# Kernel tuning notes

Measured on AMD Instinct MI355X. Metric: run time of the kernel, lower is better.

The kernel has to match this reference:

```python
import jax, jax.numpy as jnp
import numpy as np

# Hard-coded constants from the original module
GAMMA = 0.1      # self.gamma default
N_STEPS = 10     # self.n_steps default
RHO = 0.9        # RMSProp decay
LR = 0.009       # RMSProp learning rate
MOM = 0.9        # momentum
EPS = 1e-8       # RMSProp epsilon
ABS_EPS = 1e-6   # diff_abs smoothing: diff_abs(x) = sqrt(x^2 + 1e-6)

B, IN_DIM, OUT_DIM = 4096, 2048, 4096


def setup_inputs() -> dict:
    key = jax.random.key(0)
    k1, k2 = jax.random.split(key)
    inputs = jax.random.normal(k1, (B, IN_DIM), dtype=jnp.float32)
    # keras 'uniform' init: U(-0.05, 0.05), shape (output_dim, input_dim)
    W = jax.random.uniform(k2, (OUT_DIM, IN_DIM), minval=-0.05, maxval=0.05, dtype=jnp.float32)
    return {"inputs": inputs, "W": W}


def reference(inputs, W):
    batch = inputs.shape[0]
    out_dim = W.shape[0]
    a = jnp.sqrt(inputs * inputs + ABS_EPS)          # diff_abs(inputs), [B, in_dim]
    act = lambda u: 0.5 * (1.0 + jnp.exp(-u))        # self.activation

    def cost(x):
        # l1_norm.sum() + l1_inov + own_norm  (prior = 0)
        l1 = (GAMMA * act(x @ W) * a).sum()
        l1_inov = (GAMMA / 10.0) * jnp.sum(x * x)
        own = GAMMA * jnp.sum(jnp.sqrt(x * x + ABS_EPS))
        return l1 + l1_inov + own

    grad_cost = jax.grad(cost)

    def step(carry, _):
        x, acc1, acc2 = carry
        g = grad_cost(x)                              # [B, out_dim]
        new_acc1 = RHO * acc1 + (1.0 - RHO) * g * g
        denom = jnp.sqrt(new_acc1 + EPS)
        new_acc2 = MOM * acc2 - LR * g / denom
        cand = x - LR * g / denom
        t = 0.1 * LR / denom                          # elementwise prox threshold
        new_x = jnp.maximum(cand - t, 0.0) + jnp.minimum(cand + t, 0.0) + MOM * new_acc2
        new_x = jax.lax.stop_gradient(new_x)          # theano disconnected_grad
        return (new_x, new_acc1, new_acc2), None

    z = jnp.zeros((batch, out_dim), dtype=inputs.dtype)
    # scan runs n_steps; last step's l1_norm uses the state after n_steps-1 updates,
    # so run n_steps-1 updates then compute the final l1_norm directly.
    (x, _, _), _ = jax.lax.scan(step, (z, z, z), None, length=N_STEPS - 1)
    return GAMMA * act(x @ W) * a                     # outputs[-1][-1]: last l1_norm, [B, in_dim]
```

## Files before the change

kernel.cpp:

```cpp
#include <hip/hip_runtime.h>
#include <cstdint>
#include <cstddef>

#define B_DIM   4096
#define IN_DIM  2048
#define OUT_DIM 4096

typedef __attribute__((ext_vector_type(8))) __bf16 bf16x8;
typedef __attribute__((ext_vector_type(4))) float  f32x4;

__device__ __forceinline__ unsigned short f2bf(float f) {
    unsigned int u = __float_as_uint(f);
    u += 0x7FFFu + ((u >> 16) & 1u);
    return (unsigned short)(u >> 16);
}
__device__ __forceinline__ float bf2f(unsigned short b) {
    return __uint_as_float(((unsigned int)b) << 16);
}

__device__ __forceinline__ void gload16(const void* g, void* l) {
    __builtin_amdgcn_global_load_lds(
        (const __attribute__((address_space(1))) void*)g,
        (__attribute__((address_space(3))) void*)l, 16, 0, 0);
}

__global__ void prep_g0_kernel(const float* __restrict__ in, unsigned short* __restrict__ Gb) {
    int i = blockIdx.x * 256 + threadIdx.x;
    float4 v = reinterpret_cast<const float4*>(in)[i];
    ushort4 g;
    g.x = f2bf(-0.05f * sqrtf(v.x * v.x + 1e-6f));
    g.y = f2bf(-0.05f * sqrtf(v.y * v.y + 1e-6f));
    g.z = f2bf(-0.05f * sqrtf(v.z * v.z + 1e-6f));
    g.w = f2bf(-0.05f * sqrtf(v.w * v.w + 1e-6f));
    reinterpret_cast<ushort4*>(Gb)[i] = g;
}

__global__ void conv_w_kernel(const float* __restrict__ W, unsigned short* __restrict__ Wb,
                              unsigned short* __restrict__ WTb) {
    __shared__ float tile[64][65];
    const int i0 = blockIdx.x * 64;
    const int j0 = blockIdx.y * 64;
    const int c  = threadIdx.x & 63;
    const int rq = threadIdx.x >> 6;
#pragma unroll
    for (int rp = 0; rp < 16; ++rp) {
        int row = rp * 4 + rq;
        float w = W[(size_t)(j0 + row) * IN_DIM + i0 + c];
        tile[row][c] = w;
        Wb[(size_t)(j0 + row) * IN_DIM + i0 + c] = f2bf(w);
    }
    __syncthreads();
#pragma unroll
    for (int rp = 0; rp < 16; ++rp) {
        int row = rp * 4 + rq;
        WTb[(size_t)(i0 + row) * OUT_DIM + j0 + c] = f2bf(tile[c][row]);
    }
}

template <int EPI>
__global__ __launch_bounds__(256, 2)
void gemm_nt(const unsigned short* __restrict__ A, const unsigned short* __restrict__ Bm,
             int N, int K,
             const float* __restrict__ inb, unsigned short* __restrict__ Gb,
             float* __restrict__ out,
             float* __restrict__ x, unsigned short* __restrict__ acc1,
             unsigned short* __restrict__ acc2, unsigned short* __restrict__ xb) {
    __shared__ alignas(16) char smem[17408];
    const int tid  = threadIdx.x;
    const int lane = tid & 63;
    const int w    = tid >> 6;
    const int nbx  = N >> 7;
    const int nwg  = gridDim.x;
    const int cpx  = nwg >> 3;
    const int bid  = (int)blockIdx.x;
    const int swz  = (bid & 7) * cpx + (bid >> 3);
    const int bx   = swz % nbx;
    const int by   = swz / nbx;
    const int row0 = by << 7;
    const int col0 = bx << 7;

    const int q     = lane >> 2;
    const int s     = lane & 3;
    const int rowS0 = w * 16 + q;
    const size_t strideK2 = (size_t)K * 2;
    const char* Ab = (const char*)A;
    const char* Bb = (const char*)Bm;
    const char* gA0 = Ab + (size_t)(row0 + rowS0)      * strideK2 + s * 16;
    const char* gA1 = Ab + (size_t)(row0 + rowS0 + 64) * strideK2 + s * 16;
    const char* gB0 = Bb + (size_t)(col0 + rowS0)      * strideK2 + s * 16;
    const char* gB1 = Bb + (size_t)(col0 + rowS0 + 64) * strideK2 + s * 16;
    char* lA0 = smem + w * 1024;
    char* lA1 = smem + 4096  + w * 1024;
    char* lB0 = smem + 8192  + w * 1024;
    char* lB1 = smem + 12288 + w * 1024;

    const int wm = w >> 1, wn = w & 1;
    int aOff[4], bOff[4];
#pragma unroll
    for (int m = 0; m < 4; ++m) {
        aOff[m] = (wm * 64 + m * 16 + (lane & 15)) * 64 + ((lane >> 4) * 16);
        bOff[m] = 8192 + (wn * 64 + m * 16 + (lane & 15)) * 64 + ((lane >> 4) * 16);
    }

    f32x4 acc[4][4] = {};

    for (int k0 = 0; k0 < K; k0 += 32) {
        const size_t kb = (size_t)k0 * 2;
        gload16(gA0 + kb, lA0);
        gload16(gA1 + kb, lA1);
        gload16(gB0 + kb, lB0);
        gload16(gB1 + kb, lB1);
        __syncthreads();
        bf16x8 aF[4], bF[4];
#pragma unroll
        for (int m = 0; m < 4; ++m) aF[m] = *reinterpret_cast<const bf16x8*>(smem + aOff[m]);
#pragma unroll
        for (int n = 0; n < 4; ++n) bF[n] = *reinterpret_cast<const bf16x8*>(smem + bOff[n]);
#pragma unroll
        for (int m = 0; m < 4; ++m)
#pragma unroll
            for (int n = 0; n < 4; ++n)
                acc[m][n] = __builtin_amdgcn_mfma_f32_16x16x32_bf16(aF[m], bF[n], acc[m][n], 0, 0, 0);
        __syncthreads();
    }

    float* lep = (float*)(smem + w * 4352);
    const int li = lane >> 4;
    const int lc = lane & 15;
    const int row0w = row0 + wm * 64;
    const int col0w = col0 + wn * 64;
#pragma unroll
    for (int m = 0; m < 4; ++m) {
#pragma unroll
        for (int n = 0; n < 4; ++n)
#pragma unroll
            for (int i = 0; i < 4; ++i)
                lep[(li * 4 + i) * 68 + n * 16 + lc] = acc[m][n][i];
#pragma unroll
        for (int rr = 0; rr < 4; ++rr) {
            const int row = rr + li * 4;
            float4 v = *reinterpret_cast<const float4*>(&lep[row * 68 + lc * 4]);
            const size_t idx  = (size_t)(row0w + m * 16 + row) * N + col0w + lc * 4;
            const size_t idx4 = idx >> 2;
            if constexpr (EPI == 0) {
                float4 iv = reinterpret_cast<const float4*>(inb)[idx4];
                ushort4 g;
                g.x = f2bf(-0.05f * sqrtf(iv.x * iv.x + 1e-6f) * expf(-v.x));
                g.y = f2bf(-0.05f * sqrtf(iv.y * iv.y + 1e-6f) * expf(-v.y));
                g.z = f2bf(-0.05f * sqrtf(iv.z * iv.z + 1e-6f) * expf(-v.z));
                g.w = f2bf(-0.05f * sqrtf(iv.w * iv.w + 1e-6f) * expf(-v.w));
                *reinterpret_cast<ushort4*>(&Gb[idx]) = g;
            } else if constexpr (EPI == 1) {
                float4 iv = reinterpret_cast<const float4*>(inb)[idx4];
                float4 o;
                o.x = 0.05f * (1.0f + expf(-v.x)) * sqrtf(iv.x * iv.x + 1e-6f);
                o.y = 0.05f * (1.0f + expf(-v.y)) * sqrtf(iv.y * iv.y + 1e-6f);
                o.z = 0.05f * (1.0f + expf(-v.z)) * sqrtf(iv.z * iv.z + 1e-6f);
                o.w = 0.05f * (1.0f + expf(-v.w)) * sqrtf(iv.w * iv.w + 1e-6f);
                reinterpret_cast<float4*>(out)[idx4] = o;
            } else {
                float4  xv  = reinterpret_cast<const float4*>(x)[idx4];
                ushort4 a1u = *reinterpret_cast<const ushort4*>(&acc1[idx]);
                ushort4 a2u = *reinterpret_cast<const ushort4*>(&acc2[idx]);
                float xs[4] = {xv.x, xv.y, xv.z, xv.w};
                float vs[4] = {v.x, v.y, v.z, v.w};
                unsigned short a1s[4] = {a1u.x, a1u.y, a1u.z, a1u.w};
                unsigned short a2s[4] = {a2u.x, a2u.y, a2u.z, a2u.w};
                float xn4[4]; unsigned short a1n[4], a2n[4], xbn[4];
#pragma unroll
                for (int j = 0; j < 4; ++j) {
                    float g    = vs[j] + 0.02f * xs[j] + 0.1f * xs[j] * rsqrtf(xs[j] * xs[j] + 1e-6f);
                    float a1   = 0.9f * bf2f(a1s[j]) + 0.1f * g * g;
                    float inv  = rsqrtf(a1 + 1e-8f);
                    float r_   = 0.009f * g * inv;
                    float a2   = 0.9f * bf2f(a2s[j]) - r_;
                    float cand = xs[j] - r_;
                    float t    = 0.0009f * inv;
                    float xn   = fmaxf(cand - t, 0.0f) + fminf(cand + t, 0.0f) + 0.9f * a2;
                    xn4[j] = xn; a1n[j] = f2bf(a1); a2n[j] = f2bf(a2); xbn[j] = f2bf(xn);
                }
                float4 xo = {xn4[0], xn4[1], xn4[2], xn4[3]};
                reinterpret_cast<float4*>(x)[idx4] = xo;
                *reinterpret_cast<ushort4*>(&acc1[idx]) = make_ushort4(a1n[0], a1n[1], a1n[2], a1n[3]);
                *reinterpret_cast<ushort4*>(&acc2[idx]) = make_ushort4(a2n[0], a2n[1], a2n[2], a2n[3]);
                *reinterpret_cast<ushort4*>(&xb[idx])   = make_ushort4(xbn[0], xbn[1], xbn[2], xbn[3]);
            }
        }
    }
}

extern "C" void kernel_launch(void* const* d_in, const int* in_sizes, int n_in,
                              void* d_out, int out_size, void* d_ws, size_t ws_size,
                              hipStream_t stream) {
    const float* in = (const float*)d_in[0];
    const float* W  = (const float*)d_in[1];
    float* out = (float*)d_out;
    char* ws = (char*)d_ws;

    float*          x    = (float*)(ws);
    unsigned short* acc1 = (unsigned short*)(ws + ((size_t)64  << 20));
    unsigned short* acc2 = (unsigned short*)(ws + ((size_t)96  << 20));
    unsigned short* xb   = (unsigned short*)(ws + ((size_t)128 << 20));
    unsigned short* Wb   = (unsigned short*)(ws + ((size_t)160 << 20));
    unsigned short* WTb  = (unsigned short*)(ws + ((size_t)176 << 20));
    unsigned short* Gb   = (unsigned short*)(ws + ((size_t)192 << 20));

    hipMemsetAsync(ws, 0, (size_t)128 << 20, stream);

    prep_g0_kernel<<<dim3(B_DIM * IN_DIM / 4 / 256), dim3(256), 0, stream>>>(in, Gb);
    conv_w_kernel<<<dim3(IN_DIM / 64, OUT_DIM / 64), dim3(256), 0, stream>>>(W, Wb, WTb);

    const int gridFwd  = (IN_DIM / 128) * (B_DIM / 128);
    const int gridGrad = (OUT_DIM / 128) * (B_DIM / 128);

    for (int step = 0; step < 9; ++step) {
        if (step > 0) {
            gemm_nt<0><<<dim3(gridFwd), dim3(256), 0, stream>>>(
                xb, WTb, IN_DIM, OUT_DIM, in, Gb, nullptr, nullptr, nullptr, nullptr, nullptr);
        }
        gemm_nt<2><<<dim3(gridGrad), dim3(256), 0, stream>>>(
            Gb, Wb, OUT_DIM, IN_DIM, nullptr, nullptr, nullptr, x, acc1, acc2, xb);
    }
    gemm_nt<1><<<dim3(gridFwd), dim3(256), 0, stream>>>(
        xb, WTb, IN_DIM, OUT_DIM, in, nullptr, out, nullptr, nullptr, nullptr, nullptr);
}
```

Before: 1.869 ms.

## Replace GEMM with larger-tile 4-stage ring-buffered pipeline using swizzled LDS

The bf16 GEMM is rewritten with 512-thread blocks and larger output tiles (128x256 forward, 256x256 grad). Global-to-LDS loads go through a 4-slot ring with prefetch three k-steps ahead and explicit vmcnt waits, replacing the old load-sync-compute-sync loop. The LDS layout is XOR-swizzled to avoid bank conflicts, and MFMA sections raise wave priority. This aims to hide memory latency and improve operand reuse, at the cost of much more LDS per block and lower occupancy.

```diff
diff --git a/kernel.cpp b/kernel.cpp
--- a/kernel.cpp
+++ b/kernel.cpp
@@ -8,13 +8,14 @@
 
 typedef __attribute__((ext_vector_type(8))) __bf16 bf16x8;
 typedef __attribute__((ext_vector_type(4))) float  f32x4;
-
-__device__ __forceinline__ unsigned short f2bf(float f) {
+typedef unsigned short ushortT;
+
+__device__ __forceinline__ ushortT f2bf(float f) {
     unsigned int u = __float_as_uint(f);
     u += 0x7FFFu + ((u >> 16) & 1u);
-    return (unsigned short)(u >> 16);
-}
-__device__ __forceinline__ float bf2f(unsigned short b) {
+    return (ushortT)(u >> 16);
+}
+__device__ __forceinline__ float bf2f(ushortT b) {
     return __uint_as_float(((unsigned int)b) << 16);
 }
 
@@ -24,7 +25,7 @@
         (__attribute__((address_space(3))) void*)l, 16, 0, 0);
 }
 
-__global__ void prep_g0_kernel(const float* __restrict__ in, unsigned short* __restrict__ Gb) {
+__global__ void prep_g0_kernel(const float* __restrict__ in, ushortT* __restrict__ Gb) {
     int i = blockIdx.x * 256 + threadIdx.x;
     float4 v = reinterpret_cast<const float4*>(in)[i];
     ushort4 g;
@@ -35,8 +36,8 @@
     reinterpret_cast<ushort4*>(Gb)[i] = g;
 }
 
-__global__ void conv_w_kernel(const float* __restrict__ W, unsigned short* __restrict__ Wb,
-                              unsigned short* __restrict__ WTb) {
+__global__ void conv_w_kernel(const float* __restrict__ W, ushortT* __restrict__ Wb,
+                              ushortT* __restrict__ WTb) {
     __shared__ float tile[64][65];
     const int i0 = blockIdx.x * 64;
     const int j0 = blockIdx.y * 64;
@@ -57,85 +58,145 @@
     }
 }
 
-template <int EPI>
-__global__ __launch_bounds__(256, 2)
-void gemm_nt(const unsigned short* __restrict__ A, const unsigned short* __restrict__ Bm,
-             int N, int K,
-             const float* __restrict__ inb, unsigned short* __restrict__ Gb,
-             float* __restrict__ out,
-             float* __restrict__ x, unsigned short* __restrict__ acc1,
-             unsigned short* __restrict__ acc2, unsigned short* __restrict__ xb) {
-    __shared__ alignas(16) char smem[17408];
+template <int EPI, int BM>
+__global__ __launch_bounds__(512, 2)
+void gemm_ring(const ushortT* __restrict__ A, const ushortT* __restrict__ Bm,
+               int N, int K,
+               const float* __restrict__ inb, ushortT* __restrict__ Gb,
+               float* __restrict__ out,
+               float* __restrict__ x, ushortT* __restrict__ acc1,
+               ushortT* __restrict__ acc2, ushortT* __restrict__ xb) {
+    constexpr int BN   = 256;
+    constexpr int ASZ  = BM * 64;
+    constexpr int BSZ  = BN * 64;
+    constexpr int SLOT = ASZ + BSZ;
+    constexpr int LA   = BM / 128;
+    constexpr int LB   = BN / 128;
+    constexpr int L    = LA + LB;
+    constexpr int MR   = BM / 32;
+    __shared__ alignas(16) char smem[4 * SLOT];
+
     const int tid  = threadIdx.x;
     const int lane = tid & 63;
     const int w    = tid >> 6;
-    const int nbx  = N >> 7;
+    const int wm   = w >> 2;
+    const int wn   = w & 3;
+    const int nbx  = N / BN;
     const int nwg  = gridDim.x;
     const int cpx  = nwg >> 3;
     const int bid  = (int)blockIdx.x;
     const int swz  = (bid & 7) * cpx + (bid >> 3);
     const int bx   = swz % nbx;
     const int by   = swz / nbx;
-    const int row0 = by << 7;
-    const int col0 = bx << 7;
-
-    const int q     = lane >> 2;
-    const int s     = lane & 3;
-    const int rowS0 = w * 16 + q;
+    const int row0 = by * BM;
+    const int col0 = bx * BN;
+
     const size_t strideK2 = (size_t)K * 2;
-    const char* Ab = (const char*)A;
-    const char* Bb = (const char*)Bm;
-    const char* gA0 = Ab + (size_t)(row0 + rowS0)      * strideK2 + s * 16;
-    const char* gA1 = Ab + (size_t)(row0 + rowS0 + 64) * strideK2 + s * 16;
-    const char* gB0 = Bb + (size_t)(col0 + rowS0)      * strideK2 + s * 16;
-    const char* gB1 = Bb + (size_t)(col0 + rowS0 + 64) * strideK2 + s * 16;
-    char* lA0 = smem + w * 1024;
-    char* lA1 = smem + 4096  + w * 1024;
-    char* lB0 = smem + 8192  + w * 1024;
-    char* lB1 = smem + 12288 + w * 1024;
-
-    const int wm = w >> 1, wn = w & 1;
-    int aOff[4], bOff[4];
-#pragma unroll
-    for (int m = 0; m < 4; ++m) {
-        aOff[m] = (wm * 64 + m * 16 + (lane & 15)) * 64 + ((lane >> 4) * 16);
-        bOff[m] = 8192 + (wn * 64 + m * 16 + (lane & 15)) * 64 + ((lane >> 4) * 16);
-    }
-
-    f32x4 acc[4][4] = {};
-
-    for (int k0 = 0; k0 < K; k0 += 32) {
-        const size_t kb = (size_t)k0 * 2;
-        gload16(gA0 + kb, lA0);
-        gload16(gA1 + kb, lA1);
-        gload16(gB0 + kb, lB0);
-        gload16(gB1 + kb, lB1);
-        __syncthreads();
+
+    const char* gAp[LA]; int lAo[LA];
+#pragma unroll
+    for (int i = 0; i < LA; ++i) {
+        int Lp  = i * 512 + tid;
+        int row = Lp >> 2, sl = Lp & 3;
+        int src = sl ^ ((row >> 1) & 3);
+        gAp[i] = (const char*)A + (size_t)(row0 + row) * strideK2 + src * 16;
+        lAo[i] = i * 8192 + w * 1024;
+    }
+    const char* gBp[LB]; int lBo[LB];
+#pragma unroll
+    for (int i = 0; i < LB; ++i) {
+        int Lp  = i * 512 + tid;
+        int row = Lp >> 2, sl = Lp & 3;
+        int src = sl ^ ((row >> 1) & 3);
+        gBp[i] = (const char*)Bm + (size_t)(col0 + row) * strideK2 + src * 16;
+        lBo[i] = ASZ + i * 8192 + w * 1024;
+    }
+    auto stage = [&](int tt) {
+        char* sb = smem + (tt & 3) * SLOT;
+        const size_t kb = (size_t)tt * 64;
+#pragma unroll
+        for (int i = 0; i < LA; ++i) gload16(gAp[i] + kb, sb + lAo[i]);
+#pragma unroll
+        for (int i = 0; i < LB; ++i) gload16(gBp[i] + kb, sb + lBo[i]);
+    };
+
+    int aRd[MR], bRd[4];
+#pragma unroll
+    for (int m = 0; m < MR; ++m) {
+        int row = wm * (BM / 2) + m * 16 + (lane & 15);
+        aRd[m] = row * 64 + (((lane >> 4) ^ ((row >> 1) & 3)) * 16);
+    }
+#pragma unroll
+    for (int n = 0; n < 4; ++n) {
+        int row = wn * 64 + n * 16 + (lane & 15);
+        bRd[n] = ASZ + row * 64 + (((lane >> 4) ^ ((row >> 1) & 3)) * 16);
+    }
+
+    f32x4 acc[MR][4] = {};
+
+    const int nt = K >> 5;
+    stage(0); stage(1); stage(2);
+
+    for (int t = 0; t < nt; ++t) {
+        __builtin_amdgcn_s_barrier();
+        if (t + 3 < nt) stage(t + 3);
+        const int rem = nt - 1 - t;
+        if constexpr (L == 4) {
+            if (rem >= 3)      asm volatile("s_waitcnt vmcnt(12)" ::: "memory");
+            else if (rem == 2) asm volatile("s_waitcnt vmcnt(8)"  ::: "memory");
+            else if (rem == 1) asm volatile("s_waitcnt vmcnt(4)"  ::: "memory");
+            else               asm volatile("s_waitcnt vmcnt(0)"  ::: "memory");
+        } else {
+            if (rem >= 3)      asm volatile("s_waitcnt vmcnt(9)"  ::: "memory");
+            else if (rem == 2) asm volatile("s_waitcnt vmcnt(6)"  ::: "memory");
+            else if (rem == 1) asm volatile("s_waitcnt vmcnt(3)"  ::: "memory");
+            else               asm volatile("s_waitcnt vmcnt(0)"  ::: "memory");
+        }
+        __builtin_amdgcn_s_barrier();
+
+        const char* sb = smem + (t & 3) * SLOT;
         bf16x8 aF[4], bF[4];
 #pragma unroll
-        for (int m = 0; m < 4; ++m) aF[m] = *reinterpret_cast<const bf16x8*>(smem + aOff[m]);
-#pragma unroll
-        for (int n = 0; n < 4; ++n) bF[n] = *reinterpret_cast<const bf16x8*>(smem + bOff[n]);
+        for (int n = 0; n < 4; ++n) bF[n] = *reinterpret_cast<const bf16x8*>(sb + bRd[n]);
+#pragma unroll
+        for (int m = 0; m < 4; ++m) aF[m] = *reinterpret_cast<const bf16x8*>(sb + aRd[m]);
+        __builtin_amdgcn_s_setprio(1);
 #pragma unroll
         for (int m = 0; m < 4; ++m)
 #pragma unroll
             for (int n = 0; n < 4; ++n)
                 acc[m][n] = __builtin_amdgcn_mfma_f32_16x16x32_bf16(aF[m], bF[n], acc[m][n], 0, 0, 0);
-        __syncthreads();
-    }
+        __builtin_amdgcn_s_setprio(0);
+        if constexpr (MR == 8) {
+            bf16x8 aG[4];
+#pragma unroll
+            for (int m = 0; m < 4; ++m) aG[m] = *reinterpret_cast<const bf16x8*>(sb + aRd[m + 4]);
+            __builtin_amdgcn_s_setprio(1);
+#pragma unroll
+            for (int m = 0; m < 4; ++m)
+#pragma unroll
+                for (int n = 0; n < 4; ++n)
+                    acc[m + 4][n] = __builtin_amdgcn_mfma_f32_16x16x32_bf16(aG[m], bF[n], acc[m + 4][n], 0, 0, 0);
+            __builtin_amdgcn_s_setprio(0);
+        }
+    }
+
+    __builtin_amdgcn_s_barrier();
 
     float* lep = (float*)(smem + w * 4352);
     const int li = lane >> 4;
     const int lc = lane & 15;
-    const int row0w = row0 + wm * 64;
+    const int row0w = row0 + wm * (BM / 2);
     const int col0w = col0 + wn * 64;
 #pragma unroll
-    for (int m = 0; m < 4; ++m) {
+    for (int m = 0; m < MR; ++m) {
 #pragma unroll
         for (int n = 0; n < 4; ++n)
 #pragma unroll
             for (int i = 0; i < 4; ++i)
                 lep[(li * 4 + i) * 68 + n * 16 + lc] = acc[m][n][i];
+        asm volatile("s_waitcnt lgkmcnt(0)" ::: "memory");
+        __builtin_amdgcn_sched_barrier(0);
 #pragma unroll
         for (int rr = 0; rr < 4; ++rr) {
             const int row = rr + li * 4;
@@ -164,9 +225,9 @@
                 ushort4 a2u = *reinterpret_cast<const ushort4*>(&acc2[idx]);
                 float xs[4] = {xv.x, xv.y, xv.z, xv.w};
                 float vs[4] = {v.x, v.y, v.z, v.w};
-                unsigned short a1s[4] = {a1u.x, a1u.y, a1u.z, a1u.w};
-                unsigned short a2s[4] = {a2u.x, a2u.y, a2u.z, a2u.w};
-                float xn4[4]; unsigned short a1n[4], a2n[4], xbn[4];
+                ushortT a1s[4] = {a1u.x, a1u.y, a1u.z, a1u.w};
+                ushortT a2s[4] = {a2u.x, a2u.y, a2u.z, a2u.w};
+                float xn4[4]; ushortT a1n[4], a2n[4], xbn[4];
 #pragma unroll
                 for (int j = 0; j < 4; ++j) {
                     float g    = vs[j] + 0.02f * xs[j] + 0.1f * xs[j] * rsqrtf(xs[j] * xs[j] + 1e-6f);
@@ -175,8 +236,8 @@
                     float r_   = 0.009f * g * inv;
                     float a2   = 0.9f * bf2f(a2s[j]) - r_;
                     float cand = xs[j] - r_;
-                    float t    = 0.0009f * inv;
-                    float xn   = fmaxf(cand - t, 0.0f) + fminf(cand + t, 0.0f) + 0.9f * a2;
+                    float t_   = 0.0009f * inv;
+                    float xn   = fmaxf(cand - t_, 0.0f) + fminf(cand + t_, 0.0f) + 0.9f * a2;
                     xn4[j] = xn; a1n[j] = f2bf(a1); a2n[j] = f2bf(a2); xbn[j] = f2bf(xn);
                 }
                 float4 xo = {xn4[0], xn4[1], xn4[2], xn4[3]};
@@ -186,6 +247,7 @@
                 *reinterpret_cast<ushort4*>(&xb[idx])   = make_ushort4(xbn[0], xbn[1], xbn[2], xbn[3]);
             }
         }
+        asm volatile("s_waitcnt lgkmcnt(0)" ::: "memory");
     }
 }
 
@@ -197,30 +259,27 @@
     float* out = (float*)d_out;
     char* ws = (char*)d_ws;
 
-    float*          x    = (float*)(ws);
-    unsigned short* acc1 = (unsigned short*)(ws + ((size_t)64  << 20));
-    unsigned short* acc2 = (unsigned short*)(ws + ((size_t)96  << 20));
-    unsigned short* xb   = (unsigned short*)(ws + ((size_t)128 << 20));
-    unsigned short* Wb   = (unsigned short*)(ws + ((size_t)160 << 20));
-    unsigned short* WTb  = (unsigned short*)(ws + ((size_t)176 << 20));
-    unsigned short* Gb   = (unsigned short*)(ws + ((size_t)192 << 20));
+    float*   x    = (float*)(ws);
+    ushortT* acc1 = (ushortT*)(ws + ((size_t)64  << 20));
+    ushortT* acc2 = (ushortT*)(ws + ((size_t)96  << 20));
+    ushortT* xb   = (ushortT*)(ws + ((size_t)128 << 20));
+    ushortT* Wb   = (ushortT*)(ws + ((size_t)160 << 20));
+    ushortT* WTb  = (ushortT*)(ws + ((size_t)176 << 20));
+    ushortT* Gb   = (ushortT*)(ws + ((size_t)192 << 20));
 
     hipMemsetAsync(ws, 0, (size_t)128 << 20, stream);
 
     prep_g0_kernel<<<dim3(B_DIM * IN_DIM / 4 / 256), dim3(256), 0, stream>>>(in, Gb);
     conv_w_kernel<<<dim3(IN_DIM / 64, OUT_DIM / 64), dim3(256), 0, stream>>>(W, Wb, WTb);
 
-    const int gridFwd  = (IN_DIM / 128) * (B_DIM / 128);
-    const int gridGrad = (OUT_DIM / 128) * (B_DIM / 128);
-
     for (int step = 0; step < 9; ++step) {
         if (step > 0) {
-            gemm_nt<0><<<dim3(gridFwd), dim3(256), 0, stream>>>(
+            gemm_ring<0, 128><<<dim3(256), dim3(512), 0, stream>>>(
                 xb, WTb, IN_DIM, OUT_DIM, in, Gb, nullptr, nullptr, nullptr, nullptr, nullptr);
         }
-        gemm_nt<2><<<dim3(gridGrad), dim3(256), 0, stream>>>(
+        gemm_ring<2, 256><<<dim3(256), dim3(512), 0, stream>>>(
             Gb, Wb, OUT_DIM, IN_DIM, nullptr, nullptr, nullptr, x, acc1, acc2, xb);
     }
-    gemm_nt<1><<<dim3(gridFwd), dim3(256), 0, stream>>>(
+    gemm_ring<1, 128><<<dim3(256), dim3(512), 0, stream>>>(
         xb, WTb, IN_DIM, OUT_DIM, in, nullptr, out, nullptr, nullptr, nullptr, nullptr);
 }
```

New measurement: 1.716 ms. 8.2% less time.
